# Kernel optimization log

Measured on AMD Instinct MI355X. Metric: run time of the kernel, lower is better.

## Reference

```python
import jax, jax.numpy as jnp
import numpy as np

N = 100000

def gcn_conv(x, src, dst, W, b, n):
    # x: [N, Fin]; src/dst: [E'] (self-loops already included); W: [Fin, Fout]
    h = x @ W  # [N, Fout]
    deg = jax.ops.segment_sum(jnp.ones_like(dst, dtype=h.dtype), dst, num_segments=n)  # [N]
    dinv = deg ** -0.5  # deg >= 1 due to self-loops
    norm = dinv[src] * dinv[dst]  # [E']
    msg = h[src] * norm[:, None]  # gather + scale, [E', Fout]
    out = jax.ops.segment_sum(msg, dst, num_segments=n)  # scatter-add to targets
    return out + b

def setup_inputs() -> dict:
    key = jax.random.key(0)
    k1, k2, k3, k4, k5, k6 = jax.random.split(key, 6)
    x = jax.random.normal(k1, (N, 128), dtype=jnp.float32)
    edge_index = jax.random.randint(k2, (2, 1600000), 0, N, dtype=jnp.int32)
    W1 = jax.random.normal(k3, (128, 64), dtype=jnp.float32) * 0.1
    b1 = jnp.zeros((64,), dtype=jnp.float32)
    W2 = jax.random.normal(k4, (64, 41), dtype=jnp.float32) * 0.1
    b2 = jnp.zeros((41,), dtype=jnp.float32)
    return {"x": x, "edge_index": edge_index, "W1": W1, "b1": b1, "W2": W2, "b2": b2}

def reference(x, edge_index, W1, b1, W2, b2):
    n = x.shape[0]
    loops = jnp.arange(n, dtype=edge_index.dtype)
    src = jnp.concatenate([edge_index[0], loops])  # add self-loops (PyG gcn_norm default)
    dst = jnp.concatenate([edge_index[1], loops])
    # dropout is identity in eval mode (self.training=False)
    h = gcn_conv(x, src, dst, W1, b1, n)
    h = jax.nn.relu(h)
    out = gcn_conv(h, src, dst, W2, b2, n)
    return out
```

## Files before the change

kernel.cpp:

```cpp
#include <hip/hip_runtime.h>


#define FIN 128
#define F1  64
#define F2  41
#define FP  64

#define BSH    8
#define BCAP   6144
#define CHUNK_P 4096

#define MT 128
#define KC 16

#define SMEM_BYTES 24576

__device__ __forceinline__ unsigned short f2bf(float f) {
    unsigned u = __builtin_bit_cast(unsigned, f);
    u += 0x7FFFu + ((u >> 16) & 1u);
    return (unsigned short)(u >> 16);
}
__device__ __forceinline__ float bf2f(unsigned short h) {
    unsigned u = ((unsigned)h) << 16;
    return __builtin_bit_cast(float, u);
}

__global__ __launch_bounds__(256) void k_partmm1(
    const int* __restrict__ src, const int* __restrict__ dst,
    unsigned short* __restrict__ offs, int* __restrict__ pairs,
    int E, int nchunks, int NB,
    const float* __restrict__ x, const float* __restrict__ W1,
    unsigned short* __restrict__ hs, int n) {
    __shared__ alignas(16) char smem[SMEM_BYTES];
    int tid = threadIdx.x;
    if ((int)blockIdx.x < nchunks) {
        int* hist = (int*)smem;
        int* lex  = hist + 512;
        int* limg = lex + 256;
        int e0  = blockIdx.x * CHUNK_P;
        int ds[CHUNK_P / 256], ss[CHUNK_P / 256];
#pragma unroll
        for (int j = 0; j < CHUNK_P / 256; j++) {
            int e = e0 + j * 256 + tid;
            if (e < E) { ds[j] = dst[e]; ss[j] = src[e]; } else ds[j] = -1;
        }
        hist[tid] = 0; hist[tid + 256] = 0;
        __syncthreads();
#pragma unroll
        for (int j = 0; j < CHUNK_P / 256; j++)
            if (ds[j] >= 0) atomicAdd(&hist[ds[j] >> BSH], 1);
        __syncthreads();
        int b0 = 2 * tid, b1 = 2 * tid + 1;
        int c0 = hist[b0], c1 = hist[b1];
        int s  = c0 + c1;
        lex[tid] = s;
        __syncthreads();
        for (int off = 1; off < 256; off <<= 1) {
            int v = lex[tid];
            int a = (tid >= off) ? lex[tid - off] : 0;
            __syncthreads();
            lex[tid] = v + a;
            __syncthreads();
        }
        int incl = lex[tid];
        int ex0 = incl - s;
        int ex1 = ex0 + c0;
        unsigned short* orow = offs + (size_t)blockIdx.x * (NB + 1);
        if (b0 < NB) orow[b0] = (unsigned short)ex0;
        if (b1 < NB) orow[b1] = (unsigned short)ex1;
        if (tid == 255) orow[NB] = (unsigned short)incl;
        hist[b0] = ex0; hist[b1] = ex1;
        __syncthreads();
#pragma unroll
        for (int j = 0; j < CHUNK_P / 256; j++) {
            if (ds[j] >= 0) {
                int b = ds[j] >> BSH;
                int p = atomicAdd(&hist[b], 1);
                limg[p] = (ss[j] << BSH) | (ds[j] & 255);
            }
        }
        __syncthreads();
        int tot = lex[255];
        int* pout = pairs + (size_t)blockIdx.x * CHUNK_P;
        for (int k = tid; k < tot; k += 256)
            pout[k] = limg[k];
    } else {
        unsigned short* Ws = (unsigned short*)smem;
        float (*As)[MT] = (float(*)[MT])(smem + FIN * F1 * 2);
        int n0 = ((int)blockIdx.x - nchunks) * MT;
#pragma unroll
        for (int j = 0; j < 8; j++) {
            int f = j * 256 + tid;
            float4 w4 = ((const float4*)W1)[f];
            ushort4 o = { f2bf(w4.x), f2bf(w4.y), f2bf(w4.z), f2bf(w4.w) };
            ((ushort4*)Ws)[f] = o;
        }
        int m0 = (tid & 15) * 8;
        int c0 = (tid >> 4) * 4;
        int m_l = tid & 127;
        int kh  = (tid >> 7) * 8;
        bool mvalid = (n0 + m_l) < n;
        const float* xrow = x + (size_t)(n0 + m_l) * FIN + kh;
        float acc[8][4] = {};
        for (int kc = 0; kc < FIN; kc += KC) {
            __syncthreads();
            float4 v0 = mvalid ? *(const float4*)(xrow + kc)     : float4{0.f,0.f,0.f,0.f};
            float4 v1 = mvalid ? *(const float4*)(xrow + kc + 4) : float4{0.f,0.f,0.f,0.f};
            As[kh + 0][m_l] = v0.x; As[kh + 1][m_l] = v0.y;
            As[kh + 2][m_l] = v0.z; As[kh + 3][m_l] = v0.w;
            As[kh + 4][m_l] = v1.x; As[kh + 5][m_l] = v1.y;
            As[kh + 6][m_l] = v1.z; As[kh + 7][m_l] = v1.w;
            __syncthreads();
#pragma unroll
            for (int k = 0; k < KC; k++) {
                float4 a0 = *(const float4*)&As[k][m0];
                float4 a1 = *(const float4*)&As[k][m0 + 4];
                ushort4 wq = *(const ushort4*)&Ws[(kc + k) * F1 + c0];
                float wx = bf2f(wq.x), wy = bf2f(wq.y);
                float wz = bf2f(wq.z), ww = bf2f(wq.w);
                float a[8] = {a0.x, a0.y, a0.z, a0.w, a1.x, a1.y, a1.z, a1.w};
#pragma unroll
                for (int i = 0; i < 8; i++) {
                    acc[i][0] += a[i] * wx;
                    acc[i][1] += a[i] * wy;
                    acc[i][2] += a[i] * wz;
                    acc[i][3] += a[i] * ww;
                }
            }
        }
#pragma unroll
        for (int i = 0; i < 8; i++) {
            int node = n0 + m0 + i;
            if (node < n) {
                ushort4 o = { f2bf(acc[i][0]), f2bf(acc[i][1]),
                              f2bf(acc[i][2]), f2bf(acc[i][3]) };
                *(ushort4*)&hs[((size_t)node << 6) + c0] = o;
            }
        }
    }
}

__global__ __launch_bounds__(256) void k_build(
    const unsigned short* __restrict__ offs, const int* __restrict__ pairs,
    int nchunks, int NB, int* __restrict__ adj,
    int2* __restrict__ rowinfo, float* __restrict__ dinv,
    unsigned short* __restrict__ hs1, int n) {
    __shared__ int lcnt[256];
    __shared__ int lex[256];
    __shared__ int lcur[256];
    __shared__ float ldv[256];
    int tid = threadIdx.x;
    int b   = blockIdx.x;
    int NB1 = NB + 1;
    int node0 = b << BSH;
    int base  = b * BCAP;

    lcnt[tid] = 0;
    __syncthreads();
    for (int c = tid; c < nchunks; c += 256) {
        int s0 = offs[(size_t)c * NB1 + b];
        int s1 = offs[(size_t)c * NB1 + b + 1];
        const int* pc = pairs + (size_t)c * CHUNK_P;
        for (int i = s0; i < s1; i++) atomicAdd(&lcnt[pc[i] & 255], 1);
    }
    __syncthreads();
    int own = lcnt[tid];
    lex[tid] = own;
    __syncthreads();
    for (int off = 1; off < 256; off <<= 1) {
        int val = lex[tid];
        int add = (tid >= off) ? lex[tid - off] : 0;
        __syncthreads();
        lex[tid] = val + add;
        __syncthreads();
    }
    int excl = lex[tid] - own;
    float dvn = rsqrtf((float)own + 1.0f);
    lcur[tid] = excl;
    ldv[tid]  = dvn;
    __syncthreads();
    for (int c = tid; c < nchunks; c += 256) {
        int s0 = offs[(size_t)c * NB1 + b];
        int s1 = offs[(size_t)c * NB1 + b + 1];
        const int* pc = pairs + (size_t)c * CHUNK_P;
        for (int i = s0; i < s1; i++) {
            int pk  = pc[i];
            int pos = atomicAdd(&lcur[pk & 255], 1);
            adj[base + pos] = pk >> BSH;
        }
    }
    int node = node0 + tid;
    if (node < n) {
        rowinfo[node] = make_int2(base + excl, own);
        dinv[node]    = dvn;
    }
    for (int u = tid; u < 2048; u += 256) {
        int nd = node0 + (u >> 3);
        if (nd >= n) break;
        float dv = ldv[u >> 3];
        ushort4* p = (ushort4*)&hs1[((size_t)nd << 6) + (u & 7) * 8];
        ushort4 a = p[0], c = p[1];
        a.x = f2bf(bf2f(a.x) * dv); a.y = f2bf(bf2f(a.y) * dv);
        a.z = f2bf(bf2f(a.z) * dv); a.w = f2bf(bf2f(a.w) * dv);
        c.x = f2bf(bf2f(c.x) * dv); c.y = f2bf(bf2f(c.y) * dv);
        c.z = f2bf(bf2f(c.z) * dv); c.w = f2bf(bf2f(c.w) * dv);
        p[0] = a; p[1] = c;
    }
}

__global__ __launch_bounds__(256) void k_agg1(
    const int2* __restrict__ rowinfo, const int* __restrict__ adj,
    const unsigned short* __restrict__ hs, const float* __restrict__ dinv,
    const float* __restrict__ b1, unsigned short* __restrict__ h1b, int n, int AT) {
    int node = blockIdx.x * 4 + (threadIdx.x >> 6);
    if (node >= n) return;
    int lane = threadIdx.x & 63;
    int grp  = lane >> 4;
    int p4   = (lane & 15) * 4;
    int2 ri = rowinfo[node];
    int beg = ri.x, deg = ri.y;
    float4 acc = {0.f, 0.f, 0.f, 0.f};
    if (grp == 0) {
        ushort4 u = *(const ushort4*)&hs[((size_t)node << 6) + p4];
        acc.x = bf2f(u.x); acc.y = bf2f(u.y); acc.z = bf2f(u.z); acc.w = bf2f(u.w);
    }
    for (int base = 0; base < deg; base += 64) {
        int m = deg - base; if (m > 64) m = 64;
        int idx = beg + base + lane;
        int myoff = adj[idx < AT ? idx : 0] << 6;
        int e = 0;
        for (; e + 16 <= m; e += 16) {
            int o0 = __shfl(myoff, e + grp),      o1 = __shfl(myoff, e + 4 + grp);
            int o2 = __shfl(myoff, e + 8 + grp),  o3 = __shfl(myoff, e + 12 + grp);
            ushort4 u0 = *(const ushort4*)&hs[(size_t)o0 + p4];
            ushort4 u1 = *(const ushort4*)&hs[(size_t)o1 + p4];
            ushort4 u2 = *(const ushort4*)&hs[(size_t)o2 + p4];
            ushort4 u3 = *(const ushort4*)&hs[(size_t)o3 + p4];
            acc.x += (bf2f(u0.x) + bf2f(u1.x)) + (bf2f(u2.x) + bf2f(u3.x));
            acc.y += (bf2f(u0.y) + bf2f(u1.y)) + (bf2f(u2.y) + bf2f(u3.y));
            acc.z += (bf2f(u0.z) + bf2f(u1.z)) + (bf2f(u2.z) + bf2f(u3.z));
            acc.w += (bf2f(u0.w) + bf2f(u1.w)) + (bf2f(u2.w) + bf2f(u3.w));
        }
        for (; e < m; e += 4) {
            int sl = e + grp;
            int o = __shfl(myoff, sl);
            if (sl < m) {
                ushort4 u = *(const ushort4*)&hs[(size_t)o + p4];
                acc.x += bf2f(u.x); acc.y += bf2f(u.y);
                acc.z += bf2f(u.z); acc.w += bf2f(u.w);
            }
        }
    }
    acc.x += __shfl_xor(acc.x, 16); acc.y += __shfl_xor(acc.y, 16);
    acc.z += __shfl_xor(acc.z, 16); acc.w += __shfl_xor(acc.w, 16);
    acc.x += __shfl_xor(acc.x, 32); acc.y += __shfl_xor(acc.y, 32);
    acc.z += __shfl_xor(acc.z, 32); acc.w += __shfl_xor(acc.w, 32);
    if (grp == 0) {
        float dvn = dinv[node];
        float4 bg = *(const float4*)&b1[p4];
        float vx = acc.x * dvn + bg.x; vx = vx > 0.f ? vx : 0.f;
        float vy = acc.y * dvn + bg.y; vy = vy > 0.f ? vy : 0.f;
        float vz = acc.z * dvn + bg.z; vz = vz > 0.f ? vz : 0.f;
        float vw = acc.w * dvn + bg.w; vw = vw > 0.f ? vw : 0.f;
        ushort4 o = { f2bf(vx), f2bf(vy), f2bf(vz), f2bf(vw) };
        *(ushort4*)&h1b[((size_t)node << 6) + p4] = o;
    }
}

__global__ __launch_bounds__(256) void k_mm2(
    const unsigned short* __restrict__ h1b, const float* __restrict__ W2,
    const float* __restrict__ dinv, unsigned short* __restrict__ hs2, int n) {
    __shared__ float Ws[F1 * FP];
    __shared__ float As[KC][MT];
    int t  = threadIdx.x;
    int n0 = blockIdx.x * MT;
    for (int idx = t; idx < F1 * FP; idx += 256) {
        int k = idx >> 6, c = idx & 63;
        Ws[idx] = (c < F2) ? W2[k * F2 + c] : 0.f;
    }
    int m0 = (t & 15) * 8;
    int c0 = (t >> 4) * 4;
    int m_l = t & 127;
    int kh  = (t >> 7) * 8;
    bool mvalid = (n0 + m_l) < n;
    const unsigned short* hrow = h1b + ((size_t)(n0 + m_l) << 6) + kh;
    float acc[8][4] = {};
    for (int kc = 0; kc < F1; kc += KC) {
        __syncthreads();
        ushort4 u0 = mvalid ? *(const ushort4*)(hrow + kc)     : ushort4{0,0,0,0};
        ushort4 u1 = mvalid ? *(const ushort4*)(hrow + kc + 4) : ushort4{0,0,0,0};
        As[kh + 0][m_l] = bf2f(u0.x); As[kh + 1][m_l] = bf2f(u0.y);
        As[kh + 2][m_l] = bf2f(u0.z); As[kh + 3][m_l] = bf2f(u0.w);
        As[kh + 4][m_l] = bf2f(u1.x); As[kh + 5][m_l] = bf2f(u1.y);
        As[kh + 6][m_l] = bf2f(u1.z); As[kh + 7][m_l] = bf2f(u1.w);
        __syncthreads();
#pragma unroll
        for (int k = 0; k < KC; k++) {
            float4 a0 = *(const float4*)&As[k][m0];
            float4 a1 = *(const float4*)&As[k][m0 + 4];
            float4 w  = *(const float4*)&Ws[(kc + k) * FP + c0];
            float a[8] = {a0.x, a0.y, a0.z, a0.w, a1.x, a1.y, a1.z, a1.w};
#pragma unroll
            for (int i = 0; i < 8; i++) {
                acc[i][0] += a[i] * w.x;
                acc[i][1] += a[i] * w.y;
                acc[i][2] += a[i] * w.z;
                acc[i][3] += a[i] * w.w;
            }
        }
    }
#pragma unroll
    for (int i = 0; i < 8; i++) {
        int node = n0 + m0 + i;
        if (node < n) {
            float dv = dinv[node];
            ushort4 o = { f2bf(acc[i][0] * dv), f2bf(acc[i][1] * dv),
                          f2bf(acc[i][2] * dv), f2bf(acc[i][3] * dv) };
            *(ushort4*)&hs2[((size_t)node << 6) + c0] = o;
        }
    }
}

__global__ __launch_bounds__(256) void k_agg2(
    const int2* __restrict__ rowinfo, const int* __restrict__ adj,
    const unsigned short* __restrict__ hs2, const float* __restrict__ dinv,
    const float* __restrict__ b2, float* __restrict__ out, int n, int AT) {
    int node = blockIdx.x * 4 + (threadIdx.x >> 6);
    if (node >= n) return;
    int lane = threadIdx.x & 63;
    int grp  = lane >> 4;
    int p4   = (lane & 15) * 4;
    int2 ri = rowinfo[node];
    int beg = ri.x, deg = ri.y;
    float4 acc = {0.f, 0.f, 0.f, 0.f};
    if (grp == 0) {
        ushort4 u = *(const ushort4*)&hs2[((size_t)node << 6) + p4];
        acc.x = bf2f(u.x); acc.y = bf2f(u.y); acc.z = bf2f(u.z); acc.w = bf2f(u.w);
    }
    for (int base = 0; base < deg; base += 64) {
        int m = deg - base; if (m > 64) m = 64;
        int idx = beg + base + lane;
        int myoff = adj[idx < AT ? idx : 0] << 6;
        int e = 0;
        for (; e + 16 <= m; e += 16) {
            int o0 = __shfl(myoff, e + grp),      o1 = __shfl(myoff, e + 4 + grp);
            int o2 = __shfl(myoff, e + 8 + grp),  o3 = __shfl(myoff, e + 12 + grp);
            ushort4 u0 = *(const ushort4*)&hs2[(size_t)o0 + p4];
            ushort4 u1 = *(const ushort4*)&hs2[(size_t)o1 + p4];
            ushort4 u2 = *(const ushort4*)&hs2[(size_t)o2 + p4];
            ushort4 u3 = *(const ushort4*)&hs2[(size_t)o3 + p4];
            acc.x += (bf2f(u0.x) + bf2f(u1.x)) + (bf2f(u2.x) + bf2f(u3.x));
            acc.y += (bf2f(u0.y) + bf2f(u1.y)) + (bf2f(u2.y) + bf2f(u3.y));
            acc.z += (bf2f(u0.z) + bf2f(u1.z)) + (bf2f(u2.z) + bf2f(u3.z));
            acc.w += (bf2f(u0.w) + bf2f(u1.w)) + (bf2f(u2.w) + bf2f(u3.w));
        }
        for (; e < m; e += 4) {
            int sl = e + grp;
            int o = __shfl(myoff, sl);
            if (sl < m) {
                ushort4 u = *(const ushort4*)&hs2[(size_t)o + p4];
                acc.x += bf2f(u.x); acc.y += bf2f(u.y);
                acc.z += bf2f(u.z); acc.w += bf2f(u.w);
            }
        }
    }
    acc.x += __shfl_xor(acc.x, 16); acc.y += __shfl_xor(acc.y, 16);
    acc.z += __shfl_xor(acc.z, 16); acc.w += __shfl_xor(acc.w, 16);
    acc.x += __shfl_xor(acc.x, 32); acc.y += __shfl_xor(acc.y, 32);
    acc.z += __shfl_xor(acc.z, 32); acc.w += __shfl_xor(acc.w, 32);
    if (grp == 0) {
        float dv = dinv[node];
        float vv[4] = {acc.x, acc.y, acc.z, acc.w};
#pragma unroll
        for (int j = 0; j < 4; j++) {
            int f = p4 + j;
            if (f < F2) out[(size_t)node * F2 + f] = vv[j] * dv + b2[f];
        }
    }
}

extern "C" void kernel_launch(void* const* d_in, const int* in_sizes, int n_in,
                              void* d_out, int out_size, void* d_ws, size_t ws_size,
                              hipStream_t stream) {
    const float* x  = (const float*)d_in[0];
    const int*   ei = (const int*)d_in[1];
    const float* W1 = (const float*)d_in[2];
    const float* b1 = (const float*)d_in[3];
    const float* W2 = (const float*)d_in[4];
    const float* b2 = (const float*)d_in[5];
    float* out = (float*)d_out;

    const int n = in_sizes[0] / FIN;
    const int E = in_sizes[1] / 2;
    const int* src = ei;
    const int* dst = ei + E;
    const int nbuck   = (n + 255) >> BSH;
    const int nchunks = (E + CHUNK_P - 1) / CHUNK_P;
    const int nmm     = (n + MT - 1) / MT;
    const int nagg    = (n + 3) / 4;
    const int adjtot  = nbuck * BCAP;

    char* ws = (char*)d_ws;
    size_t off = 0;
    auto alloc = [&](size_t bytes) {
        void* p = ws + off;
        off = (off + bytes + 511) & ~(size_t)511;
        return p;
    };
    unsigned short* offs = (unsigned short*)alloc((size_t)nchunks * (nbuck + 1) * 2);
    int*   pairs   = (int*)alloc((size_t)nchunks * CHUNK_P * 4);
    int*   adj     = (int*)alloc((size_t)adjtot * 4 + 256);
    int2*  rowinfo = (int2*)alloc((size_t)n * 8);
    float* dinv    = (float*)alloc((size_t)n * 4);
    unsigned short* hs1 = (unsigned short*)alloc((size_t)n * FP * 2);
    unsigned short* hs2 = (unsigned short*)alloc((size_t)n * FP * 2);
    unsigned short* h1b = (unsigned short*)alloc((size_t)n * FP * 2);

    k_partmm1<<<nchunks + nmm, 256, 0, stream>>>(src, dst, offs, pairs, E, nchunks,
                                                 nbuck, x, W1, hs1, n);
    k_build<<<nbuck, 256, 0, stream>>>(offs, pairs, nchunks, nbuck, adj, rowinfo,
                                       dinv, hs1, n);
    k_agg1<<<nagg, 256, 0, stream>>>(rowinfo, adj, hs1, dinv, b1, h1b, n, adjtot);
    k_mm2<<<nmm, 256, 0, stream>>>(h1b, W2, dinv, hs2, n);
    k_agg2<<<nagg, 256, 0, stream>>>(rowinfo, adj, hs2, dinv, b2, out, n, adjtot);
}
```

Baseline: 293.7 us.

## Fuse layer-1 aggregation with layer-2 matmul; widen bucket build to 1024 threads

Merges the layer-1 aggregation and the second matmul into one kernel. Each wave keeps its node's 64-wide ReLU output in shared memory and multiplies it by W2 held in LDS, so the intermediate h1b buffer is never written or re-read and one launch goes away. Separately, k_build now runs 1024 threads per block, and each chunk's pair list is scanned by a whole wave rather than a single thread, which spreads the serial per-chunk loops. The cost is that every 4-node block reloads the full W2 into LDS and adds a block-wide barrier.

```diff
diff --git a/kernel.cpp b/kernel.cpp
--- a/kernel.cpp
+++ b/kernel.cpp
@@ -140,7 +140,7 @@
     }
 }
 
-__global__ __launch_bounds__(256) void k_build(
+__global__ __launch_bounds__(1024) void k_build(
     const unsigned short* __restrict__ offs, const int* __restrict__ pairs,
     int nchunks, int NB, int* __restrict__ adj,
     int2* __restrict__ rowinfo, float* __restrict__ dinv,
@@ -149,52 +149,57 @@
     __shared__ int lex[256];
     __shared__ int lcur[256];
     __shared__ float ldv[256];
-    int tid = threadIdx.x;
-    int b   = blockIdx.x;
-    int NB1 = NB + 1;
+    int tid  = threadIdx.x;
+    int wave = tid >> 6;
+    int lane = tid & 63;
+    int b    = blockIdx.x;
+    int NB1  = NB + 1;
     int node0 = b << BSH;
     int base  = b * BCAP;
 
-    lcnt[tid] = 0;
+    if (tid < 256) lcnt[tid] = 0;
     __syncthreads();
-    for (int c = tid; c < nchunks; c += 256) {
+    for (int c = wave; c < nchunks; c += 16) {
         int s0 = offs[(size_t)c * NB1 + b];
         int s1 = offs[(size_t)c * NB1 + b + 1];
         const int* pc = pairs + (size_t)c * CHUNK_P;
-        for (int i = s0; i < s1; i++) atomicAdd(&lcnt[pc[i] & 255], 1);
+        for (int i = s0 + lane; i < s1; i += 64)
+            atomicAdd(&lcnt[pc[i] & 255], 1);
     }
     __syncthreads();
-    int own = lcnt[tid];
-    lex[tid] = own;
+    int own = (tid < 256) ? lcnt[tid] : 0;
+    if (tid < 256) lex[tid] = own;
     __syncthreads();
     for (int off = 1; off < 256; off <<= 1) {
-        int val = lex[tid];
-        int add = (tid >= off) ? lex[tid - off] : 0;
-        __syncthreads();
-        lex[tid] = val + add;
-        __syncthreads();
-    }
-    int excl = lex[tid] - own;
+        int val = 0, add = 0;
+        if (tid < 256) {
+            val = lex[tid];
+            add = (tid >= off) ? lex[tid - off] : 0;
+        }
+        __syncthreads();
+        if (tid < 256) lex[tid] = val + add;
+        __syncthreads();
+    }
+    int excl = (tid < 256) ? (lex[tid] - own) : 0;
     float dvn = rsqrtf((float)own + 1.0f);
-    lcur[tid] = excl;
-    ldv[tid]  = dvn;
+    if (tid < 256) { lcur[tid] = excl; ldv[tid] = dvn; }
     __syncthreads();
-    for (int c = tid; c < nchunks; c += 256) {
+    for (int c = wave; c < nchunks; c += 16) {
         int s0 = offs[(size_t)c * NB1 + b];
         int s1 = offs[(size_t)c * NB1 + b + 1];
         const int* pc = pairs + (size_t)c * CHUNK_P;
-        for (int i = s0; i < s1; i++) {
+        for (int i = s0 + lane; i < s1; i += 64) {
             int pk  = pc[i];
             int pos = atomicAdd(&lcur[pk & 255], 1);
             adj[base + pos] = pk >> BSH;
         }
     }
     int node = node0 + tid;
-    if (node < n) {
+    if (tid < 256 && node < n) {
         rowinfo[node] = make_int2(base + excl, own);
         dinv[node]    = dvn;
     }
-    for (int u = tid; u < 2048; u += 256) {
+    for (int u = tid; u < 2048; u += 1024) {
         int nd = node0 + (u >> 3);
         if (nd >= n) break;
         float dv = ldv[u >> 3];
@@ -208,116 +213,86 @@
     }
 }
 
-__global__ __launch_bounds__(256) void k_agg1(
+__global__ __launch_bounds__(256) void k_agg1mm2(
     const int2* __restrict__ rowinfo, const int* __restrict__ adj,
     const unsigned short* __restrict__ hs, const float* __restrict__ dinv,
-    const float* __restrict__ b1, unsigned short* __restrict__ h1b, int n, int AT) {
-    int node = blockIdx.x * 4 + (threadIdx.x >> 6);
-    if (node >= n) return;
-    int lane = threadIdx.x & 63;
+    const float* __restrict__ b1, const float* __restrict__ W2,
+    unsigned short* __restrict__ hs2, int n, int AT) {
+    __shared__ float W2s[F1 * FP];
+    __shared__ float H[4][F1];
+    int tid  = threadIdx.x;
+    int w    = tid >> 6;
+    int node = blockIdx.x * 4 + w;
+    int lane = tid & 63;
     int grp  = lane >> 4;
     int p4   = (lane & 15) * 4;
-    int2 ri = rowinfo[node];
-    int beg = ri.x, deg = ri.y;
-    float4 acc = {0.f, 0.f, 0.f, 0.f};
-    if (grp == 0) {
-        ushort4 u = *(const ushort4*)&hs[((size_t)node << 6) + p4];
-        acc.x = bf2f(u.x); acc.y = bf2f(u.y); acc.z = bf2f(u.z); acc.w = bf2f(u.w);
-    }
-    for (int base = 0; base < deg; base += 64) {
-        int m = deg - base; if (m > 64) m = 64;
-        int idx = beg + base + lane;
-        int myoff = adj[idx < AT ? idx : 0] << 6;
-        int e = 0;
-        for (; e + 16 <= m; e += 16) {
-            int o0 = __shfl(myoff, e + grp),      o1 = __shfl(myoff, e + 4 + grp);
-            int o2 = __shfl(myoff, e + 8 + grp),  o3 = __shfl(myoff, e + 12 + grp);
-            ushort4 u0 = *(const ushort4*)&hs[(size_t)o0 + p4];
-            ushort4 u1 = *(const ushort4*)&hs[(size_t)o1 + p4];
-            ushort4 u2 = *(const ushort4*)&hs[(size_t)o2 + p4];
-            ushort4 u3 = *(const ushort4*)&hs[(size_t)o3 + p4];
-            acc.x += (bf2f(u0.x) + bf2f(u1.x)) + (bf2f(u2.x) + bf2f(u3.x));
-            acc.y += (bf2f(u0.y) + bf2f(u1.y)) + (bf2f(u2.y) + bf2f(u3.y));
-            acc.z += (bf2f(u0.z) + bf2f(u1.z)) + (bf2f(u2.z) + bf2f(u3.z));
-            acc.w += (bf2f(u0.w) + bf2f(u1.w)) + (bf2f(u2.w) + bf2f(u3.w));
-        }
-        for (; e < m; e += 4) {
-            int sl = e + grp;
-            int o = __shfl(myoff, sl);
-            if (sl < m) {
-                ushort4 u = *(const ushort4*)&hs[(size_t)o + p4];
-                acc.x += bf2f(u.x); acc.y += bf2f(u.y);
-                acc.z += bf2f(u.z); acc.w += bf2f(u.w);
-            }
-        }
-    }
-    acc.x += __shfl_xor(acc.x, 16); acc.y += __shfl_xor(acc.y, 16);
-    acc.z += __shfl_xor(acc.z, 16); acc.w += __shfl_xor(acc.w, 16);
-    acc.x += __shfl_xor(acc.x, 32); acc.y += __shfl_xor(acc.y, 32);
-    acc.z += __shfl_xor(acc.z, 32); acc.w += __shfl_xor(acc.w, 32);
-    if (grp == 0) {
-        float dvn = dinv[node];
-        float4 bg = *(const float4*)&b1[p4];
-        float vx = acc.x * dvn + bg.x; vx = vx > 0.f ? vx : 0.f;
-        float vy = acc.y * dvn + bg.y; vy = vy > 0.f ? vy : 0.f;
-        float vz = acc.z * dvn + bg.z; vz = vz > 0.f ? vz : 0.f;
-        float vw = acc.w * dvn + bg.w; vw = vw > 0.f ? vw : 0.f;
-        ushort4 o = { f2bf(vx), f2bf(vy), f2bf(vz), f2bf(vw) };
-        *(ushort4*)&h1b[((size_t)node << 6) + p4] = o;
-    }
-}
-
-__global__ __launch_bounds__(256) void k_mm2(
-    const unsigned short* __restrict__ h1b, const float* __restrict__ W2,
-    const float* __restrict__ dinv, unsigned short* __restrict__ hs2, int n) {
-    __shared__ float Ws[F1 * FP];
-    __shared__ float As[KC][MT];
-    int t  = threadIdx.x;
-    int n0 = blockIdx.x * MT;
-    for (int idx = t; idx < F1 * FP; idx += 256) {
+    for (int idx = tid; idx < F1 * FP; idx += 256) {
         int k = idx >> 6, c = idx & 63;
-        Ws[idx] = (c < F2) ? W2[k * F2 + c] : 0.f;
-    }
-    int m0 = (t & 15) * 8;
-    int c0 = (t >> 4) * 4;
-    int m_l = t & 127;
-    int kh  = (t >> 7) * 8;
-    bool mvalid = (n0 + m_l) < n;
-    const unsigned short* hrow = h1b + ((size_t)(n0 + m_l) << 6) + kh;
-    float acc[8][4] = {};
-    for (int kc = 0; kc < F1; kc += KC) {
-        __syncthreads();
-        ushort4 u0 = mvalid ? *(const ushort4*)(hrow + kc)     : ushort4{0,0,0,0};
-        ushort4 u1 = mvalid ? *(const ushort4*)(hrow + kc + 4) : ushort4{0,0,0,0};
-        As[kh + 0][m_l] = bf2f(u0.x); As[kh + 1][m_l] = bf2f(u0.y);
-        As[kh + 2][m_l] = bf2f(u0.z); As[kh + 3][m_l] = bf2f(u0.w);
-        As[kh + 4][m_l] = bf2f(u1.x); As[kh + 5][m_l] = bf2f(u1.y);
-        As[kh + 6][m_l] = bf2f(u1.z); As[kh + 7][m_l] = bf2f(u1.w);
-        __syncthreads();
-#pragma unroll
-        for (int k = 0; k < KC; k++) {
-            float4 a0 = *(const float4*)&As[k][m0];
-            float4 a1 = *(const float4*)&As[k][m0 + 4];
-            float4 w  = *(const float4*)&Ws[(kc + k) * FP + c0];
-            float a[8] = {a0.x, a0.y, a0.z, a0.w, a1.x, a1.y, a1.z, a1.w};
-#pragma unroll
-            for (int i = 0; i < 8; i++) {
-                acc[i][0] += a[i] * w.x;
-                acc[i][1] += a[i] * w.y;
-                acc[i][2] += a[i] * w.z;
-                acc[i][3] += a[i] * w.w;
-            }
-        }
-    }
-#pragma unroll
-    for (int i = 0; i < 8; i++) {
-        int node = n0 + m0 + i;
-        if (node < n) {
-            float dv = dinv[node];
-            ushort4 o = { f2bf(acc[i][0] * dv), f2bf(acc[i][1] * dv),
-                          f2bf(acc[i][2] * dv), f2bf(acc[i][3] * dv) };
-            *(ushort4*)&hs2[((size_t)node << 6) + c0] = o;
-        }
+        W2s[idx] = (c < F2) ? W2[k * F2 + c] : 0.f;
+    }
+    if (node < n) {
+        int2 ri = rowinfo[node];
+        int beg = ri.x, deg = ri.y;
+        float4 acc = {0.f, 0.f, 0.f, 0.f};
+        if (grp == 0) {
+            ushort4 u = *(const ushort4*)&hs[((size_t)node << 6) + p4];
+            acc.x = bf2f(u.x); acc.y = bf2f(u.y); acc.z = bf2f(u.z); acc.w = bf2f(u.w);
+        }
+        for (int base = 0; base < deg; base += 64) {
+            int m = deg - base; if (m > 64) m = 64;
+            int idx = beg + base + lane;
+            int myoff = adj[idx < AT ? idx : 0] << 6;
+            int e = 0;
+            for (; e + 16 <= m; e += 16) {
+                int o0 = __shfl(myoff, e + grp),      o1 = __shfl(myoff, e + 4 + grp);
+                int o2 = __shfl(myoff, e + 8 + grp),  o3 = __shfl(myoff, e + 12 + grp);
+                ushort4 u0 = *(const ushort4*)&hs[(size_t)o0 + p4];
+                ushort4 u1 = *(const ushort4*)&hs[(size_t)o1 + p4];
+                ushort4 u2 = *(const ushort4*)&hs[(size_t)o2 + p4];
+                ushort4 u3 = *(const ushort4*)&hs[(size_t)o3 + p4];
+                acc.x += (bf2f(u0.x) + bf2f(u1.x)) + (bf2f(u2.x) + bf2f(u3.x));
+                acc.y += (bf2f(u0.y) + bf2f(u1.y)) + (bf2f(u2.y) + bf2f(u3.y));
+                acc.z += (bf2f(u0.z) + bf2f(u1.z)) + (bf2f(u2.z) + bf2f(u3.z));
+                acc.w += (bf2f(u0.w) + bf2f(u1.w)) + (bf2f(u2.w) + bf2f(u3.w));
+            }
+            for (; e < m; e += 4) {
+                int sl = e + grp;
+                int o = __shfl(myoff, sl);
+                if (sl < m) {
+                    ushort4 u = *(const ushort4*)&hs[(size_t)o + p4];
+                    acc.x += bf2f(u.x); acc.y += bf2f(u.y);
+                    acc.z += bf2f(u.z); acc.w += bf2f(u.w);
+                }
+            }
+        }
+        acc.x += __shfl_xor(acc.x, 16); acc.y += __shfl_xor(acc.y, 16);
+        acc.z += __shfl_xor(acc.z, 16); acc.w += __shfl_xor(acc.w, 16);
+        acc.x += __shfl_xor(acc.x, 32); acc.y += __shfl_xor(acc.y, 32);
+        acc.z += __shfl_xor(acc.z, 32); acc.w += __shfl_xor(acc.w, 32);
+        if (grp == 0) {
+            float dvn = dinv[node];
+            float4 bg = *(const float4*)&b1[p4];
+            float vx = acc.x * dvn + bg.x; vx = vx > 0.f ? vx : 0.f;
+            float vy = acc.y * dvn + bg.y; vy = vy > 0.f ? vy : 0.f;
+            float vz = acc.z * dvn + bg.z; vz = vz > 0.f ? vz : 0.f;
+            float vw = acc.w * dvn + bg.w; vw = vw > 0.f ? vw : 0.f;
+            H[w][p4 + 0] = vx; H[w][p4 + 1] = vy;
+            H[w][p4 + 2] = vz; H[w][p4 + 3] = vw;
+        }
+    }
+    __syncthreads();
+    if (node < n) {
+        int c = lane;
+        float s = 0.f;
+#pragma unroll
+        for (int k = 0; k < F1; k += 4) {
+            float4 hv = *(const float4*)&H[w][k];
+            s += hv.x * W2s[(k + 0) * FP + c];
+            s += hv.y * W2s[(k + 1) * FP + c];
+            s += hv.z * W2s[(k + 2) * FP + c];
+            s += hv.w * W2s[(k + 3) * FP + c];
+        }
+        hs2[((size_t)node << 6) + c] = f2bf(s * dinv[node]);
     }
 }
 
@@ -414,13 +389,12 @@
     float* dinv    = (float*)alloc((size_t)n * 4);
     unsigned short* hs1 = (unsigned short*)alloc((size_t)n * FP * 2);
     unsigned short* hs2 = (unsigned short*)alloc((size_t)n * FP * 2);
-    unsigned short* h1b = (unsigned short*)alloc((size_t)n * FP * 2);
 
     k_partmm1<<<nchunks + nmm, 256, 0, stream>>>(src, dst, offs, pairs, E, nchunks,
                                                  nbuck, x, W1, hs1, n);
-    k_build<<<nbuck, 256, 0, stream>>>(offs, pairs, nchunks, nbuck, adj, rowinfo,
-                                       dinv, hs1, n);
-    k_agg1<<<nagg, 256, 0, stream>>>(rowinfo, adj, hs1, dinv, b1, h1b, n, adjtot);
-    k_mm2<<<nmm, 256, 0, stream>>>(h1b, W2, dinv, hs2, n);
+    k_build<<<nbuck, 1024, 0, stream>>>(offs, pairs, nchunks, nbuck, adj, rowinfo,
+                                        dinv, hs1, n);
+    k_agg1mm2<<<nagg, 256, 0, stream>>>(rowinfo, adj, hs1, dinv, b1, W2, hs2,
+                                        n, adjtot);
     k_agg2<<<nagg, 256, 0, stream>>>(rowinfo, adj, hs2, dinv, b2, out, n, adjtot);
 }
```

Result: slower. 326.8 us (+11.3%).
